# Performance work log

Hardware: AMD Instinct MI355X
Metric: run time of the kernel (lower is better)

The kernel has to match this reference:

```python
import jax, jax.numpy as jnp
import numpy as np


def setup_inputs() -> dict:
    key = jax.random.key(0)
    k1, k2, k3, k4 = jax.random.split(key, 4)
    N, E, IN, OUT = 100000, 1600000, 256, 32
    feat = jax.random.normal(k1, (N, IN), dtype=jnp.float32)
    src = jax.random.randint(k2, (E,), 0, N, dtype=jnp.int64)
    dst = jax.random.randint(k3, (E,), 0, N, dtype=jnp.int64)
    weight = jax.random.normal(k4, (IN, OUT), dtype=jnp.float32) * (6.0 / (IN + OUT)) ** 0.5
    bias = jnp.zeros((OUT,), dtype=jnp.float32)
    return {"feat": feat, "src": src, "dst": dst, "weight": weight, "bias": bias}


def reference(feat, src, dst, weight, bias):
    N = feat.shape[0]
    ones = jnp.ones(src.shape[0], dtype=feat.dtype)
    # norm='both': scale sources by out_degree^-0.5
    out_deg = jnp.clip(jax.ops.segment_sum(ones, src, num_segments=N), 1.0)
    feat = feat * (out_deg ** -0.5)[:, None]
    # in_feats (256) > out_feats (32): apply weight before aggregation
    feat = feat @ weight
    # SpMM: copy_src + sum over destination nodes
    rst = jax.ops.segment_sum(feat[src], dst, num_segments=N)  # [N, out]
    # scale destinations by in_degree^-0.5
    in_deg = jnp.clip(jax.ops.segment_sum(ones, dst, num_segments=N), 1.0)
    rst = rst * (in_deg ** -0.5)[:, None]
    rst = rst + bias
    return jax.nn.relu(rst)
```

## Files before the change

### kernel.cpp

```cpp
#include <hip/hip_runtime.h>
#include <hip/hip_bf16.h>


#define IN_F 256
#define OUT_F 32

#define G_ROWS 128
#define G_BK 16
#define W_ROWS 32
#define G_NT (IN_F / G_BK)

#define BSHIFT 7
#define BNODES 128
#define NBK 1024
#define PB_EDGES 8192
#define AGG_CAP 4096
#define SLAB 8192

__device__ __forceinline__ unsigned short f2bf(float x) {
  unsigned u = __float_as_uint(x);
  unsigned r = (u + 0x7FFFu + ((u >> 16) & 1u)) >> 16;
  return (unsigned short)r;
}
__device__ __forceinline__ float bf2f(unsigned short b) {
  return __uint_as_float((unsigned)b << 16);
}


__global__ __launch_bounds__(1024) void partition_fused_kernel(
    const int* __restrict__ src, const int* __restrict__ dst,
    int* __restrict__ curS, int* __restrict__ curD,
    unsigned char* __restrict__ pairs_s, unsigned* __restrict__ pairs,
    int E, int npb) {
  __shared__ unsigned sbuf[PB_EDGES];
  __shared__ int hist[NBK];
  __shared__ int lbase[NBK + 1];
  __shared__ int gbase[NBK];
  __shared__ int wsum[16];

  int tid = threadIdx.x;
  bool isDst = (int)blockIdx.x >= npb;
  int pb = isDst ? (int)blockIdx.x - npb : (int)blockIdx.x;
  hist[tid] = 0;
  __syncthreads();

  int e0 = pb * PB_EDGES + tid * 8;
  int myb[8], myslot[8];
  unsigned mypk[8];
  unsigned char mylow[8];
  if (!isDst) {
    if (e0 + 8 <= E) {
      int4 a0 = ((const int4*)(src + e0))[0], a1 = ((const int4*)(src + e0))[1];
      int ss[8] = {a0.x, a0.y, a0.z, a0.w, a1.x, a1.y, a1.z, a1.w};
#pragma unroll
      for (int j = 0; j < 8; ++j) {
        int b = ss[j] >> BSHIFT;
        myb[j] = b;
        mylow[j] = (unsigned char)(ss[j] & (BNODES - 1));
        myslot[j] = atomicAdd(&hist[b], 1);
      }
    } else {
#pragma unroll
      for (int j = 0; j < 8; ++j) {
        int e = e0 + j;
        if (e < E) {
          int s = src[e];
          int b = s >> BSHIFT;
          myb[j] = b;
          mylow[j] = (unsigned char)(s & (BNODES - 1));
          myslot[j] = atomicAdd(&hist[b], 1);
        } else {
          myb[j] = -1;
        }
      }
    }
  } else {
    if (e0 + 8 <= E) {
      int4 a0 = ((const int4*)(src + e0))[0], a1 = ((const int4*)(src + e0))[1];
      int4 b0 = ((const int4*)(dst + e0))[0], b1 = ((const int4*)(dst + e0))[1];
      int ss[8] = {a0.x, a0.y, a0.z, a0.w, a1.x, a1.y, a1.z, a1.w};
      int dd[8] = {b0.x, b0.y, b0.z, b0.w, b1.x, b1.y, b1.z, b1.w};
#pragma unroll
      for (int j = 0; j < 8; ++j) {
        int b = dd[j] >> BSHIFT;
        myb[j] = b;
        mypk[j] = (unsigned)ss[j] | ((unsigned)(dd[j] & (BNODES - 1)) << 17);
        myslot[j] = atomicAdd(&hist[b], 1);
      }
    } else {
#pragma unroll
      for (int j = 0; j < 8; ++j) {
        int e = e0 + j;
        if (e < E) {
          int s = src[e], d = dst[e];
          int b = d >> BSHIFT;
          myb[j] = b;
          mypk[j] = (unsigned)s | ((unsigned)(d & (BNODES - 1)) << 17);
          myslot[j] = atomicAdd(&hist[b], 1);
        } else {
          myb[j] = -1;
        }
      }
    }
  }
  __syncthreads();

  {
    int v = hist[tid];
    int x = v;
#pragma unroll
    for (int d = 1; d < 64; d <<= 1) {
      int y = __shfl_up(x, d, 64);
      if ((tid & 63) >= d) x += y;
    }
    if ((tid & 63) == 63) wsum[tid >> 6] = x;
    __syncthreads();
    int off = 0;
#pragma unroll
    for (int w = 0; w < 16; ++w)
      if (w < (tid >> 6)) off += wsum[w];
    lbase[tid] = off + x - v;
    if (tid == NBK - 1) lbase[NBK] = off + x;
    if (v > 0) {
      int* cur = isDst ? curD : curS;
      int old = atomicAdd(&cur[tid], v);
      gbase[tid] = tid * SLAB + old;
    }
  }
  __syncthreads();

  if (!isDst) {
    unsigned char* sbuf8 = (unsigned char*)sbuf;
#pragma unroll
    for (int j = 0; j < 8; ++j)
      if (myb[j] >= 0) sbuf8[lbase[myb[j]] + myslot[j]] = mylow[j];
  } else {
#pragma unroll
    for (int j = 0; j < 8; ++j)
      if (myb[j] >= 0) sbuf[lbase[myb[j]] + myslot[j]] = mypk[j];
  }
  __syncthreads();

  int total = lbase[NBK];
  int idx = tid * 8;
  if (idx < total) {
    int lo = 0, hi = NBK;
    while (hi - lo > 1) {
      int mid = (lo + hi) >> 1;
      if (lbase[mid] <= idx) lo = mid; else hi = mid;
    }
    int b = lo;
    if (!isDst) {
      unsigned char* sbuf8 = (unsigned char*)sbuf;
#pragma unroll
      for (int j = 0; j < 8; ++j, ++idx) {
        if (idx >= total) break;
        while (idx >= lbase[b + 1]) ++b;
        pairs_s[gbase[b] + (idx - lbase[b])] = sbuf8[idx];
      }
    } else {
#pragma unroll
      for (int j = 0; j < 8; ++j, ++idx) {
        if (idx >= total) break;
        while (idx >= lbase[b + 1]) ++b;
        pairs[gbase[b] + (idx - lbase[b])] = sbuf[idx];
      }
    }
  }
}

__global__ __launch_bounds__(256) void src_count_kernel(
    const unsigned char* __restrict__ pairs_s, const int* __restrict__ cntS,
    float* __restrict__ scale_out, int N) {
  __shared__ int hist[BNODES];
  int tid = threadIdx.x;
  int b = blockIdx.x;
  if (tid < BNODES) hist[tid] = 0;
  __syncthreads();
  int s = b * SLAB, e = s + cntS[b];
  for (int i = s + tid; i < e; i += 256) atomicAdd(&hist[pairs_s[i]], 1);
  __syncthreads();
  if (tid < BNODES) {
    int node = (b << BSHIFT) + tid;
    if (node < N) {
      int c = hist[tid];
      scale_out[node] = (c < 1) ? 1.f : rsqrtf((float)c);
    }
  }
}

__global__ __launch_bounds__(256, 4) void gemm_kernel(
    const float* __restrict__ feat, const float* __restrict__ W,
    const float* __restrict__ scale_out, unsigned short* __restrict__ h,
    int N) {
  __shared__ float sW[IN_F * OUT_F];
  __shared__ float sF[4][2][W_ROWS * G_BK];
  __shared__ float sScale[G_ROWS];

  int tid = threadIdx.x;
  int wv = tid >> 6;
  int lane = tid & 63;
  {
    const float4* W4 = (const float4*)W;
    float4* sW4 = (float4*)sW;
#pragma unroll
    for (int i = 0; i < 8; ++i) sW4[tid + i * 256] = W4[tid + i * 256];
  }
  int grow = blockIdx.x * G_ROWS;
  if (tid < G_ROWS) {
    int gr = grow + tid;
    sScale[tid] = (gr < N) ? scale_out[gr] : 0.f;
  }
  int wrow0 = grow + wv * W_ROWS;

  auto stage = [&](int t) {
    int k0 = t * G_BK;
    float* dstb = &sF[wv][t & 1][0];
#pragma unroll
    for (int q = 0; q < 2; ++q) {
      int r = q * 16 + (lane >> 2);
      int c = (lane & 3) ^ (r & 3);
      int g = wrow0 + r;
      if (g >= N) g = N - 1;
      const float* gp = feat + (size_t)g * IN_F + k0 + c * 4;
      __builtin_amdgcn_global_load_lds(
          (const __attribute__((address_space(1))) unsigned int*)gp,
          (__attribute__((address_space(3))) unsigned int*)(dstb + q * 256 + lane * 4),
          16, 0, 0);
    }
  };

  stage(0);

  int tr = lane >> 3;
  int cg = (lane & 7) * 4;

  float acc[4][4];
#pragma unroll
  for (int i = 0; i < 4; ++i)
#pragma unroll
    for (int c = 0; c < 4; ++c) acc[i][c] = 0.f;

  __syncthreads();

  for (int t = 0; t < G_NT; ++t) {
    if (t + 1 < G_NT) {
      stage(t + 1);
      asm volatile("s_waitcnt vmcnt(2)" ::: "memory");
    } else {
      asm volatile("s_waitcnt vmcnt(0)" ::: "memory");
    }

    const float* sf = &sF[wv][t & 1][0];
    int kb = t * G_BK;
#pragma unroll
    for (int cc = 0; cc < 4; ++cc) {
      float4 a[4];
#pragma unroll
      for (int i = 0; i < 4; ++i) {
        int r = tr + 8 * i;
        a[i] = *(const float4*)(sf + r * 16 + ((cc ^ (r & 3)) << 2));
      }
#pragma unroll
      for (int j = 0; j < 4; ++j) {
        float4 w = *(const float4*)(sW + (kb + cc * 4 + j) * OUT_F + cg);
#pragma unroll
        for (int i = 0; i < 4; ++i) {
          float aj = (j == 0) ? a[i].x : (j == 1) ? a[i].y
                   : (j == 2) ? a[i].z : a[i].w;
          acc[i][0] = fmaf(aj, w.x, acc[i][0]);
          acc[i][1] = fmaf(aj, w.y, acc[i][1]);
          acc[i][2] = fmaf(aj, w.z, acc[i][2]);
          acc[i][3] = fmaf(aj, w.w, acc[i][3]);
        }
      }
    }
  }

#pragma unroll
  for (int i = 0; i < 4; ++i) {
    int r = tr + 8 * i;
    int g = wrow0 + r;
    if (g < N) {
      float s = sScale[wv * W_ROWS + r];
      ushort4 o;
      o.x = f2bf(acc[i][0] * s);
      o.y = f2bf(acc[i][1] * s);
      o.z = f2bf(acc[i][2] * s);
      o.w = f2bf(acc[i][3] * s);
      *(ushort4*)(h + (size_t)g * OUT_F + cg) = o;
    }
  }
}

__global__ __launch_bounds__(256) void sort_agg_kernel(
    const unsigned* __restrict__ pairs, const int* __restrict__ cntD,
    const unsigned short* __restrict__ h, const float* __restrict__ bias,
    float* __restrict__ out, int N) {
  __shared__ unsigned spk[AGG_CAP];
  __shared__ int hist[BNODES];
  __shared__ int rs[BNODES + 1];
  __shared__ int wsum2[4];

  int tid = threadIdx.x;
  int lane = tid & 31;
  int eg = tid >> 5;
  int b = blockIdx.x;
  int start = b * SLAB;
  int end = start + cntD[b];

  float acc[16];
  int degc[16];
#pragma unroll
  for (int t = 0; t < 16; ++t) { acc[t] = 0.f; degc[t] = 0; }

  for (int chunk = start; chunk < end; chunk += AGG_CAP) {
    int cnt = min(end - chunk, AGG_CAP);
    if (tid < BNODES) hist[tid] = 0;
    __syncthreads();

    unsigned mypk[16];
    int myslot[16];
    int nmine = 0;
    for (int i = tid; i < cnt; i += 256) {
      unsigned pk = pairs[chunk + i];
      mypk[nmine] = pk;
      myslot[nmine] = atomicAdd(&hist[pk >> 17], 1);
      ++nmine;
    }
    __syncthreads();

    {
      int v = (tid < BNODES) ? hist[tid] : 0;
      int x = v;
#pragma unroll
      for (int d = 1; d < 64; d <<= 1) {
        int y = __shfl_up(x, d, 64);
        if ((tid & 63) >= d) x += y;
      }
      if ((tid & 63) == 63) wsum2[tid >> 6] = x;
      __syncthreads();
      int off = (tid >= 64 && tid < BNODES) ? wsum2[0] : 0;
      if (tid < BNODES) rs[tid] = off + x - v;
      if (tid == BNODES - 1) rs[BNODES] = off + x;
    }
    __syncthreads();

    for (int i = 0; i < nmine; ++i) {
      unsigned pk = mypk[i];
      spk[rs[pk >> 17] + myslot[i]] = pk;
    }
    __syncthreads();

#pragma unroll 1
    for (int t = 0; t < 16; ++t) {
      int n = eg * 16 + t;
      int a = rs[n], bnd = rs[n + 1];
      degc[t] += bnd - a;
      float s = acc[t];
      int j = a;
      for (; j + 8 <= bnd; j += 8) {
        unsigned p0 = spk[j], p1 = spk[j + 1], p2 = spk[j + 2], p3 = spk[j + 3];
        unsigned p4 = spk[j + 4], p5 = spk[j + 5], p6 = spk[j + 6], p7 = spk[j + 7];
        float f0 = bf2f(h[(size_t)(p0 & 0x1FFFF) * OUT_F + lane]);
        float f1 = bf2f(h[(size_t)(p1 & 0x1FFFF) * OUT_F + lane]);
        float f2 = bf2f(h[(size_t)(p2 & 0x1FFFF) * OUT_F + lane]);
        float f3 = bf2f(h[(size_t)(p3 & 0x1FFFF) * OUT_F + lane]);
        float f4 = bf2f(h[(size_t)(p4 & 0x1FFFF) * OUT_F + lane]);
        float f5 = bf2f(h[(size_t)(p5 & 0x1FFFF) * OUT_F + lane]);
        float f6 = bf2f(h[(size_t)(p6 & 0x1FFFF) * OUT_F + lane]);
        float f7 = bf2f(h[(size_t)(p7 & 0x1FFFF) * OUT_F + lane]);
        s += ((f0 + f1) + (f2 + f3)) + ((f4 + f5) + (f6 + f7));
      }
      if (j + 4 <= bnd) {
        unsigned p0 = spk[j], p1 = spk[j + 1], p2 = spk[j + 2], p3 = spk[j + 3];
        float f0 = bf2f(h[(size_t)(p0 & 0x1FFFF) * OUT_F + lane]);
        float f1 = bf2f(h[(size_t)(p1 & 0x1FFFF) * OUT_F + lane]);
        float f2 = bf2f(h[(size_t)(p2 & 0x1FFFF) * OUT_F + lane]);
        float f3 = bf2f(h[(size_t)(p3 & 0x1FFFF) * OUT_F + lane]);
        s += (f0 + f1) + (f2 + f3);
        j += 4;
      }
      for (; j < bnd; ++j)
        s += bf2f(h[(size_t)(spk[j] & 0x1FFFF) * OUT_F + lane]);
      acc[t] = s;
    }
    __syncthreads();
  }

  int node0 = b << BSHIFT;
#pragma unroll
  for (int t = 0; t < 16; ++t) {
    int node = node0 + eg * 16 + t;
    if (node < N) {
      float sc = degc[t] > 0 ? rsqrtf((float)degc[t]) : 1.f;
      out[(size_t)node * OUT_F + lane] = fmaxf(fmaf(acc[t], sc, bias[lane]), 0.f);
    }
  }
}

__global__ __launch_bounds__(256) void degree_kernel(
    const int* __restrict__ src, const int* __restrict__ dst,
    int* __restrict__ cnt_out, int* __restrict__ cnt_in, int E) {
  int i = blockIdx.x * 256 + threadIdx.x;
  if (i < E) {
    atomicAdd(cnt_out + src[i], 1);
    atomicAdd(cnt_in + dst[i], 1);
  }
}

__global__ __launch_bounds__(256) void cnt_to_scale_kernel(
    const int* __restrict__ cnt, float* __restrict__ scale, int N) {
  int i = blockIdx.x * 256 + threadIdx.x;
  if (i < N) {
    int c = cnt[i];
    scale[i] = (c < 1) ? 1.f : rsqrtf((float)c);
  }
}

__global__ __launch_bounds__(256) void aggregate_kernel(
    const int* __restrict__ src, const int* __restrict__ dst,
    const unsigned short* __restrict__ h, float* __restrict__ out, int E) {
  int lane = threadIdx.x & 31;
  int e = (blockIdx.x * 256 + threadIdx.x) >> 5;
  if (e >= E) return;
  float v = bf2f(h[(size_t)src[e] * OUT_F + lane]);
  unsafeAtomicAdd(out + (size_t)dst[e] * OUT_F + lane, v);
}

__global__ __launch_bounds__(256) void finalize_kernel(
    float* __restrict__ out, const int* __restrict__ cnt_in,
    const float* __restrict__ bias, int N) {
  int idx = blockIdx.x * 256 + threadIdx.x;
  if (idx >= N * 8) return;
  int n = idx >> 3;
  int o = (idx & 7) * 4;
  float dg = (float)cnt_in[n];
  float s = dg < 1.f ? 1.f : rsqrtf(dg);
  float4 bv = *(const float4*)(bias + o);
  float4 v = ((const float4*)out)[idx];
  v.x = fmaxf(fmaf(v.x, s, bv.x), 0.f);
  v.y = fmaxf(fmaf(v.y, s, bv.y), 0.f);
  v.z = fmaxf(fmaf(v.z, s, bv.z), 0.f);
  v.w = fmaxf(fmaf(v.w, s, bv.w), 0.f);
  ((float4*)out)[idx] = v;
}

extern "C" void kernel_launch(void* const* d_in, const int* in_sizes, int n_in,
                              void* d_out, int out_size, void* d_ws, size_t ws_size,
                              hipStream_t stream) {
  const float* feat = (const float*)d_in[0];
  const int* src = (const int*)d_in[1];
  const int* dst = (const int*)d_in[2];
  const float* weight = (const float*)d_in[3];
  const float* bias = (const float*)d_in[4];
  float* out = (float*)d_out;

  int N = in_sizes[0] / IN_F;
  int E = in_sizes[1];
  int nb = (N + BNODES - 1) >> BSHIFT;
  int npb = (E + PB_EDGES - 1) / PB_EDGES;

  unsigned short* h = (unsigned short*)d_ws;
  unsigned* pairs = (unsigned*)(h + (size_t)N * OUT_F);
  unsigned char* pairs_s =
      (unsigned char*)(pairs + (size_t)NBK * SLAB);
  int* curS = (int*)(pairs_s + (size_t)NBK * SLAB);
  int* curD = curS + NBK;
  float* scale_out = (float*)(curD + NBK);

  size_t need = (size_t)N * OUT_F * 2 + (size_t)NBK * SLAB * 5 +
                2 * NBK * 4 + (size_t)N * 4;
  bool fast = (ws_size >= need) && (N <= (1 << 17)) && (nb <= NBK) &&
              ((size_t)E <= (size_t)3072 * nb);

  if (fast) {
    hipMemsetAsync(curS, 0, 2 * NBK * sizeof(int), stream);
    partition_fused_kernel<<<2 * npb, 1024, 0, stream>>>(
        src, dst, curS, curD, pairs_s, pairs, E, npb);
    src_count_kernel<<<nb, 256, 0, stream>>>(pairs_s, curS, scale_out, N);
    gemm_kernel<<<(N + G_ROWS - 1) / G_ROWS, 256, 0, stream>>>(
        feat, weight, scale_out, h, N);
    sort_agg_kernel<<<nb, 256, 0, stream>>>(pairs, curD, h, bias, out, N);
  } else {
    int* cnt_out = (int*)(h + (size_t)N * OUT_F);
    int* cnt_in = cnt_out + N;
    hipMemsetAsync(cnt_out, 0, (size_t)2 * N * sizeof(int), stream);
    hipMemsetAsync(out, 0, (size_t)N * OUT_F * sizeof(float), stream);
    degree_kernel<<<(E + 255) / 256, 256, 0, stream>>>(src, dst, cnt_out, cnt_in, E);
    cnt_to_scale_kernel<<<(N + 255) / 256, 256, 0, stream>>>(
        cnt_out, (float*)cnt_out, N);
    gemm_kernel<<<(N + G_ROWS - 1) / G_ROWS, 256, 0, stream>>>(
        feat, weight, (const float*)cnt_out, h, N);
    aggregate_kernel<<<(E + 7) / 8, 256, 0, stream>>>(src, dst, h, out, E);
    finalize_kernel<<<(N * 8 + 255) / 256, 256, 0, stream>>>(out, cnt_in, bias, N);
  }
}
```

Baseline: 254.1 us.

## Restructure GEMM to one row per lane with uniform weight loads; vectorize src histogram

The GEMM kernel drops the shared-memory copy of the weight matrix. Each lane now computes a full 32-wide output row, and weights are read through uniform (scalar/constant-cache) global loads, using 128-thread blocks of two waves with 64 rows each. This removes the 32KB LDS weight staging and its per-block load, which should raise occupancy. The cost is 32 accumulators per thread and an unswizzled LDS read pattern that may cause bank conflicts. The source-degree histogram now reads four byte-indices per 32-bit load to cut load instructions.

```diff
diff --git a/kernel.cpp b/kernel.cpp
--- a/kernel.cpp
+++ b/kernel.cpp
@@ -6,9 +6,6 @@
 #define OUT_F 32
 
 #define G_ROWS 128
-#define G_BK 16
-#define W_ROWS 32
-#define G_NT (IN_F / G_BK)
 
 #define BSHIFT 7
 #define BNODES 128
@@ -177,8 +174,17 @@
   int b = blockIdx.x;
   if (tid < BNODES) hist[tid] = 0;
   __syncthreads();
-  int s = b * SLAB, e = s + cntS[b];
-  for (int i = s + tid; i < e; i += 256) atomicAdd(&hist[pairs_s[i]], 1);
+  int s = b * SLAB;
+  int cnt = cntS[b];
+  int vec = cnt & ~3;
+  for (int i = tid * 4; i < vec; i += 1024) {
+    unsigned v = *(const unsigned*)(pairs_s + s + i);
+    atomicAdd(&hist[v & 255u], 1);
+    atomicAdd(&hist[(v >> 8) & 255u], 1);
+    atomicAdd(&hist[(v >> 16) & 255u], 1);
+    atomicAdd(&hist[v >> 24], 1);
+  }
+  if (tid < cnt - vec) atomicAdd(&hist[pairs_s[s + vec + tid]], 1);
   __syncthreads();
   if (tid < BNODES) {
     int node = (b << BSHIFT) + tid;
@@ -189,106 +195,81 @@
   }
 }
 
-__global__ __launch_bounds__(256, 4) void gemm_kernel(
+__global__ __launch_bounds__(128) void gemm_kernel(
     const float* __restrict__ feat, const float* __restrict__ W,
     const float* __restrict__ scale_out, unsigned short* __restrict__ h,
     int N) {
-  __shared__ float sW[IN_F * OUT_F];
-  __shared__ float sF[4][2][W_ROWS * G_BK];
-  __shared__ float sScale[G_ROWS];
+  __shared__ float sF[2][2][64 * 16];
 
   int tid = threadIdx.x;
   int wv = tid >> 6;
   int lane = tid & 63;
-  {
-    const float4* W4 = (const float4*)W;
-    float4* sW4 = (float4*)sW;
-#pragma unroll
-    for (int i = 0; i < 8; ++i) sW4[tid + i * 256] = W4[tid + i * 256];
-  }
-  int grow = blockIdx.x * G_ROWS;
-  if (tid < G_ROWS) {
-    int gr = grow + tid;
-    sScale[tid] = (gr < N) ? scale_out[gr] : 0.f;
-  }
-  int wrow0 = grow + wv * W_ROWS;
+  int wrow0 = blockIdx.x * G_ROWS + wv * 64;
+  int myrow = wrow0 + lane;
+  int rowc = myrow < N ? myrow : N - 1;
 
   auto stage = [&](int t) {
-    int k0 = t * G_BK;
     float* dstb = &sF[wv][t & 1][0];
-#pragma unroll
-    for (int q = 0; q < 2; ++q) {
-      int r = q * 16 + (lane >> 2);
-      int c = (lane & 3) ^ (r & 3);
-      int g = wrow0 + r;
+    int k0 = t * 16;
+#pragma unroll
+    for (int q = 0; q < 4; ++q) {
+      int p = q * 64 + lane;
+      int g = wrow0 + (p >> 2);
       if (g >= N) g = N - 1;
-      const float* gp = feat + (size_t)g * IN_F + k0 + c * 4;
+      const float* gp = feat + (size_t)g * IN_F + k0 + (p & 3) * 4;
       __builtin_amdgcn_global_load_lds(
           (const __attribute__((address_space(1))) unsigned int*)gp,
-          (__attribute__((address_space(3))) unsigned int*)(dstb + q * 256 + lane * 4),
+          (__attribute__((address_space(3))) unsigned int*)(dstb + p * 4),
           16, 0, 0);
     }
   };
 
+  float acc[32];
+#pragma unroll
+  for (int c = 0; c < 32; ++c) acc[c] = 0.f;
+
   stage(0);
 
-  int tr = lane >> 3;
-  int cg = (lane & 7) * 4;
-
-  float acc[4][4];
-#pragma unroll
-  for (int i = 0; i < 4; ++i)
-#pragma unroll
-    for (int c = 0; c < 4; ++c) acc[i][c] = 0.f;
-
-  __syncthreads();
-
-  for (int t = 0; t < G_NT; ++t) {
-    if (t + 1 < G_NT) {
+  for (int t = 0; t < 16; ++t) {
+    if (t + 1 < 16) {
       stage(t + 1);
-      asm volatile("s_waitcnt vmcnt(2)" ::: "memory");
+      asm volatile("s_waitcnt vmcnt(4)" ::: "memory");
     } else {
       asm volatile("s_waitcnt vmcnt(0)" ::: "memory");
     }
 
     const float* sf = &sF[wv][t & 1][0];
-    int kb = t * G_BK;
-#pragma unroll
-    for (int cc = 0; cc < 4; ++cc) {
-      float4 a[4];
-#pragma unroll
-      for (int i = 0; i < 4; ++i) {
-        int r = tr + 8 * i;
-        a[i] = *(const float4*)(sf + r * 16 + ((cc ^ (r & 3)) << 2));
-      }
+    int kb = t * 16;
+#pragma unroll
+    for (int kk = 0; kk < 4; ++kk) {
+      float4 a4 = *(const float4*)(sf + lane * 16 + kk * 4);
 #pragma unroll
       for (int j = 0; j < 4; ++j) {
-        float4 w = *(const float4*)(sW + (kb + cc * 4 + j) * OUT_F + cg);
-#pragma unroll
-        for (int i = 0; i < 4; ++i) {
-          float aj = (j == 0) ? a[i].x : (j == 1) ? a[i].y
-                   : (j == 2) ? a[i].z : a[i].w;
-          acc[i][0] = fmaf(aj, w.x, acc[i][0]);
-          acc[i][1] = fmaf(aj, w.y, acc[i][1]);
-          acc[i][2] = fmaf(aj, w.z, acc[i][2]);
-          acc[i][3] = fmaf(aj, w.w, acc[i][3]);
+        float aj = (j == 0) ? a4.x : (j == 1) ? a4.y : (j == 2) ? a4.z : a4.w;
+        const float* wrow = W + (size_t)(kb + kk * 4 + j) * OUT_F;
+#pragma unroll
+        for (int c4 = 0; c4 < 8; ++c4) {
+          float4 w = *(const float4*)(wrow + c4 * 4);
+          acc[c4 * 4 + 0] = fmaf(aj, w.x, acc[c4 * 4 + 0]);
+          acc[c4 * 4 + 1] = fmaf(aj, w.y, acc[c4 * 4 + 1]);
+          acc[c4 * 4 + 2] = fmaf(aj, w.z, acc[c4 * 4 + 2]);
+          acc[c4 * 4 + 3] = fmaf(aj, w.w, acc[c4 * 4 + 3]);
         }
       }
     }
   }
 
-#pragma unroll
-  for (int i = 0; i < 4; ++i) {
-    int r = tr + 8 * i;
-    int g = wrow0 + r;
-    if (g < N) {
-      float s = sScale[wv * W_ROWS + r];
+  float sc = scale_out[rowc];
+  if (myrow < N) {
+    unsigned short* hp = h + (size_t)myrow * OUT_F;
+#pragma unroll
+    for (int c4 = 0; c4 < 8; ++c4) {
       ushort4 o;
-      o.x = f2bf(acc[i][0] * s);
-      o.y = f2bf(acc[i][1] * s);
-      o.z = f2bf(acc[i][2] * s);
-      o.w = f2bf(acc[i][3] * s);
-      *(ushort4*)(h + (size_t)g * OUT_F + cg) = o;
+      o.x = f2bf(acc[c4 * 4 + 0] * sc);
+      o.y = f2bf(acc[c4 * 4 + 1] * sc);
+      o.z = f2bf(acc[c4 * 4 + 2] * sc);
+      o.w = f2bf(acc[c4 * 4 + 3] * sc);
+      *(ushort4*)(hp + c4 * 4) = o;
     }
   }
 }
@@ -479,7 +460,7 @@
     partition_fused_kernel<<<2 * npb, 1024, 0, stream>>>(
         src, dst, curS, curD, pairs_s, pairs, E, npb);
     src_count_kernel<<<nb, 256, 0, stream>>>(pairs_s, curS, scale_out, N);
-    gemm_kernel<<<(N + G_ROWS - 1) / G_ROWS, 256, 0, stream>>>(
+    gemm_kernel<<<(N + G_ROWS - 1) / G_ROWS, 128, 0, stream>>>(
         feat, weight, scale_out, h, N);
     sort_agg_kernel<<<nb, 256, 0, stream>>>(pairs, curD, h, bias, out, N);
   } else {
@@ -490,7 +471,7 @@
     degree_kernel<<<(E + 255) / 256, 256, 0, stream>>>(src, dst, cnt_out, cnt_in, E);
     cnt_to_scale_kernel<<<(N + 255) / 256, 256, 0, stream>>>(
         cnt_out, (float*)cnt_out, N);
-    gemm_kernel<<<(N + G_ROWS - 1) / G_ROWS, 256, 0, stream>>>(
+    gemm_kernel<<<(N + G_ROWS - 1) / G_ROWS, 128, 0, stream>>>(
         feat, weight, (const float*)cnt_out, h, N);
     aggregate_kernel<<<(E + 7) / 8, 256, 0, stream>>>(src, dst, h, out, E);
     finalize_kernel<<<(N * 8 + 255) / 256, 256, 0, stream>>>(out, cnt_in, bias, N);
```

Measured after the change: 290.4 us. +14.3%, slower.
